# Performance work log

Measured on AMD Instinct MI355X. Metric: run time of the kernel, lower is better.

## Reference

```python
import jax, jax.numpy as jnp
import numpy as np

NUM_RBF = 64
CUTOFF = 5.0
N_GRAPHS = 64


def _rbf_expand(d):
    # Gaussian RBF expansion on [0, CUTOFF] with cosine cutoff envelope.
    mus = jnp.linspace(0.0, CUTOFF, NUM_RBF, dtype=d.dtype)  # [M]
    gamma = (NUM_RBF / CUTOFF) ** 2  # 1 / spacing^2
    fc = 0.5 * (jnp.cos(jnp.pi * d / CUTOFF) + 1.0) * (d < CUTOFF)  # [E]
    return jnp.exp(-gamma * (d[:, None] - mus[None, :]) ** 2) * fc[:, None]  # [E,M]


def setup_inputs() -> dict:
    key = jax.random.key(0)
    k0, k1, k2, k3, k4, k5 = jax.random.split(key, 6)
    N, E, T = 50000, 1600000, 25
    pos = jax.random.normal(k0, (N, 3), jnp.float32) * 3.0
    edge_index = jax.random.randint(k1, (2, E), 0, N)
    atom_types = jax.random.randint(k2, (N,), 0, T)
    batch = jnp.sort(jax.random.randint(k3, (N,), 0, N_GRAPHS))
    rbf_params = jax.random.normal(k4, (T, T, NUM_RBF), jnp.float32)
    radial_filters = jax.random.uniform(k5, (T, T, NUM_RBF), jnp.float32)
    return {
        "pos": pos,
        "rbf_params": rbf_params,
        "radial_filters": radial_filters,
        "edge_index": edge_index,
        "atom_types": atom_types,
        "batch": batch,
    }


def reference(pos, rbf_params, radial_filters, edge_index, atom_types, batch):
    src, dst = edge_index[0], edge_index[1]
    # distances (no cell shifts)
    diff = pos[dst] - pos[src]                       # [E,3]
    d = jnp.sqrt(jnp.sum(diff * diff, axis=-1) + 1e-12)  # [E]
    # type-pair lookup with canonical ordering (sender <= receiver)
    s = atom_types[src]
    r = atom_types[dst]
    lo = jnp.minimum(s, r)
    hi = jnp.maximum(s, r)
    params = rbf_params[lo, hi]        # [E,M]
    filt = radial_filters[lo, hi]      # [E,M] (already in [0,1])
    expn = _rbf_expand(d) * filt       # filtered RBF expansion
    e_edge = jnp.sum(expn * params, axis=1)  # [E]
    # reduce per-edge energies to per-graph energies
    bmap = batch[src]
    energy = jax.ops.segment_sum(e_edge, bmap, num_segments=N_GRAPHS)  # [G]
    return energy
```

## Files before the change

### kernel.cpp

```cpp
#include <hip/hip_runtime.h>
#include <math.h>

#define NUM_RBF 64
#define N_GRAPHS 64

typedef int   int4v   __attribute__((ext_vector_type(4)));
typedef float float4v __attribute__((ext_vector_type(4)));


__global__ __launch_bounds__(256) void prologue_kernel(
    const float4v* __restrict__ p, const float4v* __restrict__ f,
    float4v* __restrict__ C, int n4,
    const float* __restrict__ pos, const int* __restrict__ types,
    const int* __restrict__ batch, float4v* __restrict__ rec, int N)
{
    int i = blockIdx.x * blockDim.x + threadIdx.x;
    if (i < n4) C[i] = p[i] * f[i];
    if (i < N) {
        int bits = (types[i] & 0xFF) | ((batch[i] & 0xFF) << 8);
        float4v r = { pos[3 * i], pos[3 * i + 1], pos[3 * i + 2],
                      __int_as_float(bits) };
        rec[i] = r;
    }
}

#define CUTOFF_F      5.0f
#define GAMMA_F       163.84f
#define SPACING_F     (float)(5.0 / 63.0)
#define INV_SPACING_F (float)(63.0 / 5.0)
#define PI_OVER_C_F   (float)(3.14159265358979323846 / 5.0)
#define TWO_GAMMA_S_F (float)(2.0 * 163.84 * 5.0 / 63.0)
#define LN_V          (-(64.0 / 63.0) * (64.0 / 63.0))
#define V_1           (float)exp(LN_V)
#define V_2           (float)exp(2.0 * LN_V)

__device__ __forceinline__ void edge_body(
    float4v rs, float4v rd, const float4v* __restrict__ C4, int T,
    float* __restrict__ bins)
{
    const float dx = rd.x - rs.x;
    const float dy = rd.y - rs.y;
    const float dz = rd.z - rs.z;
    const float d  = sqrtf(dx * dx + dy * dy + dz * dz + 1e-12f);
    if (d >= CUTOFF_F) return;

    const int sb = __float_as_int(rs.w);
    const int db = __float_as_int(rd.w);
    const int ts = sb & 0xFF;
    const int td = db & 0xFF;
    const int lo = min(ts, td);
    const int hi = max(ts, td);
    const int base = (lo * T + hi) * NUM_RBF;

    const float c = d * INV_SPACING_F;
    int a0 = ((int)floorf(c - 3.5f)) & ~3;
    a0 = max(0, min(NUM_RBF - 12, a0));

    const float4v* w = C4 + ((base + a0) >> 2);
    const float4v w0 = w[0], w1 = w[1], w2 = w[2];

    const float delta = d - (float)a0 * SPACING_F;
    const float d5 = delta - 5.0f * SPACING_F;
    const float t5 = __expf(-GAMMA_F * d5 * d5);
    const float x  = TWO_GAMMA_S_F * d5;
    const float u  = __expf(x);
    const float ui = __expf(-x);

    float acc = w1.y * t5;
    float t = t5, m = u * V_1;
    t *= m;  acc += w1.z * t;  m *= V_2;
    t *= m;  acc += w1.w * t;  m *= V_2;
    t *= m;  acc += w2.x * t;  m *= V_2;
    t *= m;  acc += w2.y * t;  m *= V_2;
    t *= m;  acc += w2.z * t;  m *= V_2;
    t *= m;  acc += w2.w * t;
    t = t5;  m = ui * V_1;
    t *= m;  acc += w1.x * t;  m *= V_2;
    t *= m;  acc += w0.w * t;  m *= V_2;
    t *= m;  acc += w0.z * t;  m *= V_2;
    t *= m;  acc += w0.y * t;  m *= V_2;
    t *= m;  acc += w0.x * t;

    const float fc = 0.5f * (__cosf(PI_OVER_C_F * d) + 1.0f);
    atomicAdd(&bins[(sb >> 8) & 0xFF], acc * fc);
}

__global__ __launch_bounds__(256) void edge_energy_kernel(
    const int*     __restrict__ edge_index,
    const float4v* __restrict__ rec,
    const float4v* __restrict__ C4,
    float*         __restrict__ partial,
    int E, int T)
{
    __shared__ float bins[N_GRAPHS];
    for (int i = threadIdx.x; i < N_GRAPHS; i += blockDim.x) bins[i] = 0.0f;
    __syncthreads();

    const int nfull  = E >> 2;
    const int stride = gridDim.x * blockDim.x;
    const int gid    = blockIdx.x * blockDim.x + threadIdx.x;

    for (int q = gid; q < nfull; q += stride) {
        const int e0 = q << 2;
        const int4v sv = __builtin_nontemporal_load(
            (const int4v*)(edge_index + e0));
        const int4v tv = __builtin_nontemporal_load(
            (const int4v*)(edge_index + E + e0));

        const float4v rs0 = rec[sv.x], rd0 = rec[tv.x];
        const float4v rs1 = rec[sv.y], rd1 = rec[tv.y];
        const float4v rs2 = rec[sv.z], rd2 = rec[tv.z];
        const float4v rs3 = rec[sv.w], rd3 = rec[tv.w];

        edge_body(rs0, rd0, C4, T, bins);
        edge_body(rs1, rd1, C4, T, bins);
        edge_body(rs2, rd2, C4, T, bins);
        edge_body(rs3, rd3, C4, T, bins);
    }

    if (gid == 0) {
        for (int e = nfull << 2; e < E; ++e) {
            const float4v rs = rec[edge_index[e]];
            const float4v rd = rec[edge_index[E + e]];
            edge_body(rs, rd, C4, T, bins);
        }
    }

    __syncthreads();
    for (int i = threadIdx.x; i < N_GRAPHS; i += blockDim.x)
        partial[blockIdx.x * N_GRAPHS + i] = bins[i];
}

__global__ __launch_bounds__(256) void reduce_kernel(
    const float* __restrict__ partial, float* __restrict__ out, int nblocks)
{
    const int g = blockIdx.x;
    float s = 0.0f;
    for (int i = threadIdx.x; i < nblocks; i += blockDim.x)
        s += partial[i * N_GRAPHS + g];

    for (int off = 32; off > 0; off >>= 1)
        s += __shfl_down(s, off, 64);

    __shared__ float red[4];
    const int wave = threadIdx.x >> 6;
    const int lane = threadIdx.x & 63;
    if (lane == 0) red[wave] = s;
    __syncthreads();
    if (threadIdx.x == 0)
        out[g] = red[0] + red[1] + red[2] + red[3];
}

extern "C" void kernel_launch(void* const* d_in, const int* in_sizes, int n_in,
                              void* d_out, int out_size, void* d_ws, size_t ws_size,
                              hipStream_t stream) {
    const float* pos            = (const float*)d_in[0];
    const float* rbf_params     = (const float*)d_in[1];
    const float* radial_filters = (const float*)d_in[2];
    const int*   edge_index     = (const int*)d_in[3];
    const int*   atom_types     = (const int*)d_in[4];
    const int*   batch          = (const int*)d_in[5];
    float*       out            = (float*)d_out;

    const int E = in_sizes[3] / 2;
    const int N = in_sizes[4];
    int T = 1;
    while ((T + 1) * (T + 1) * NUM_RBF <= in_sizes[1]) ++T;
    const int tbl_elems = T * T * NUM_RBF;

    float*   Ctab    = (float*)d_ws;
    float4v* recs    = (float4v*)((char*)d_ws + ((size_t)tbl_elems * 4 + 255) / 256 * 256);
    float*   partial = (float*)((char*)recs + (size_t)N * 16);

    const int nq = E >> 2;
    int nblocks = (nq + 255) / 256;
    const size_t part_off = (size_t)((char*)partial - (char*)d_ws);
    const size_t avail = (ws_size > part_off) ? (ws_size - part_off) : 0;
    const int maxb = (int)(avail / (N_GRAPHS * sizeof(float)));
    if (nblocks > maxb) nblocks = maxb > 0 ? maxb : 1;
    if (nblocks < 1) nblocks = 1;

    const int pro_n = max(tbl_elems / 4, N);
    prologue_kernel<<<(pro_n + 255) / 256, 256, 0, stream>>>(
        (const float4v*)rbf_params, (const float4v*)radial_filters,
        (float4v*)Ctab, tbl_elems / 4, pos, atom_types, batch, recs, N);
    edge_energy_kernel<<<nblocks, 256, 0, stream>>>(
        edge_index, recs, (const float4v*)Ctab, partial, E, T);
    reduce_kernel<<<N_GRAPHS, 256, 0, stream>>>(partial, out, nblocks);
}
```

Measured before the change: 94.91 us.

## Compact in-cutoff edges into shared-memory queue before RBF evaluation

The edge loop is split into two phases. Each thread first computes squared distances and pushes the surviving edges (d² < cutoff²) into an LDS queue, using a wave ballot, mbcnt prefix and one atomic per wave. Then all 256 threads evaluate the RBF window densely from that queue. The aim is to remove lane divergence, since only a fraction of edges pass the cutoff. The cost is extra block-wide barriers per iteration, LDS traffic, and a packed type-pair/graph metadata format that assumes T*T < 1024 and fewer than 64 graphs.

```diff
diff --git a/kernel.cpp b/kernel.cpp
--- a/kernel.cpp
+++ b/kernel.cpp
@@ -3,6 +3,7 @@
 
 #define NUM_RBF 64
 #define N_GRAPHS 64
+#define QCAP     1032
 
 typedef int   int4v   __attribute__((ext_vector_type(4)));
 typedef float float4v __attribute__((ext_vector_type(4)));
@@ -24,7 +25,7 @@
     }
 }
 
-#define CUTOFF_F      5.0f
+#define CUTOFF2_F     25.0f
 #define GAMMA_F       163.84f
 #define SPACING_F     (float)(5.0 / 63.0)
 #define INV_SPACING_F (float)(63.0 / 5.0)
@@ -34,23 +35,13 @@
 #define V_1           (float)exp(LN_V)
 #define V_2           (float)exp(2.0 * LN_V)
 
-__device__ __forceinline__ void edge_body(
-    float4v rs, float4v rd, const float4v* __restrict__ C4, int T,
+__device__ __forceinline__ void window_body(
+    float d2, int meta, const float4v* __restrict__ C4,
     float* __restrict__ bins)
 {
-    const float dx = rd.x - rs.x;
-    const float dy = rd.y - rs.y;
-    const float dz = rd.z - rs.z;
-    const float d  = sqrtf(dx * dx + dy * dy + dz * dz + 1e-12f);
-    if (d >= CUTOFF_F) return;
-
-    const int sb = __float_as_int(rs.w);
-    const int db = __float_as_int(rd.w);
-    const int ts = sb & 0xFF;
-    const int td = db & 0xFF;
-    const int lo = min(ts, td);
-    const int hi = max(ts, td);
-    const int base = (lo * T + hi) * NUM_RBF;
+    const float d    = sqrtf(d2);
+    const int   base = (meta & 1023) << 6;
+    const int   bin  = meta >> 10;
 
     const float c = d * INV_SPACING_F;
     int a0 = ((int)floorf(c - 3.5f)) & ~3;
@@ -82,7 +73,39 @@
     t *= m;  acc += w0.x * t;
 
     const float fc = 0.5f * (__cosf(PI_OVER_C_F * d) + 1.0f);
-    atomicAdd(&bins[(sb >> 8) & 0xFF], acc * fc);
+    atomicAdd(&bins[bin], acc * fc);
+}
+
+__device__ __forceinline__ void push_body(
+    float4v rs, float4v rd, int T,
+    float* __restrict__ qd, int* __restrict__ qm, int* __restrict__ qcnt)
+{
+    const float dx = rd.x - rs.x;
+    const float dy = rd.y - rs.y;
+    const float dz = rd.z - rs.z;
+    const float d2 = dx * dx + dy * dy + dz * dz + 1e-12f;
+    const bool alive = d2 < CUTOFF2_F;
+
+    const unsigned long long mask = __ballot(alive);
+    if (alive) {
+        const int sb = __float_as_int(rs.w);
+        const int ts = sb & 0xFF;
+        const int td = __float_as_int(rd.w) & 0xFF;
+        const int lo = min(ts, td);
+        const int hi = max(ts, td);
+        const int meta = (lo * T + hi) | (((sb >> 8) & 0x3F) << 10);
+
+        const int prefix = __builtin_amdgcn_mbcnt_hi(
+            (unsigned)(mask >> 32),
+            __builtin_amdgcn_mbcnt_lo((unsigned)mask, 0));
+        const int first = __ffsll((unsigned long long)mask) - 1;
+        int off = 0;
+        if (((int)(threadIdx.x & 63)) == first)
+            off = atomicAdd(qcnt, (int)__popcll(mask));
+        off = __shfl(off, first, 64);
+        qd[off + prefix] = d2;
+        qm[off + prefix] = meta;
+    }
 }
 
 __global__ __launch_bounds__(256) void edge_energy_kernel(
@@ -93,41 +116,65 @@
     int E, int T)
 {
     __shared__ float bins[N_GRAPHS];
-    for (int i = threadIdx.x; i < N_GRAPHS; i += blockDim.x) bins[i] = 0.0f;
+    __shared__ float qd[QCAP];
+    __shared__ int   qm[QCAP];
+    __shared__ int   qcnt;
+
+    const int tid = threadIdx.x;
+    for (int i = tid; i < N_GRAPHS; i += blockDim.x) bins[i] = 0.0f;
+    if (tid == 0) qcnt = 0;
     __syncthreads();
 
-    const int nfull  = E >> 2;
-    const int stride = gridDim.x * blockDim.x;
-    const int gid    = blockIdx.x * blockDim.x + threadIdx.x;
-
-    for (int q = gid; q < nfull; q += stride) {
-        const int e0 = q << 2;
-        const int4v sv = __builtin_nontemporal_load(
-            (const int4v*)(edge_index + e0));
-        const int4v tv = __builtin_nontemporal_load(
-            (const int4v*)(edge_index + E + e0));
-
-        const float4v rs0 = rec[sv.x], rd0 = rec[tv.x];
-        const float4v rs1 = rec[sv.y], rd1 = rec[tv.y];
-        const float4v rs2 = rec[sv.z], rd2 = rec[tv.z];
-        const float4v rs3 = rec[sv.w], rd3 = rec[tv.w];
-
-        edge_body(rs0, rd0, C4, T, bins);
-        edge_body(rs1, rd1, C4, T, bins);
-        edge_body(rs2, rd2, C4, T, bins);
-        edge_body(rs3, rd3, C4, T, bins);
-    }
-
-    if (gid == 0) {
+    const int nfull = E >> 2;
+
+    if (blockIdx.x == 0 && tid == 0) {
         for (int e = nfull << 2; e < E; ++e) {
             const float4v rs = rec[edge_index[e]];
             const float4v rd = rec[edge_index[E + e]];
-            edge_body(rs, rd, C4, T, bins);
+            const float dx = rd.x - rs.x, dy = rd.y - rs.y, dz = rd.z - rs.z;
+            const float d2 = dx * dx + dy * dy + dz * dz + 1e-12f;
+            if (d2 < CUTOFF2_F) {
+                const int sb = __float_as_int(rs.w);
+                const int ts = sb & 0xFF;
+                const int td = __float_as_int(rd.w) & 0xFF;
+                const int meta = (min(ts, td) * T + max(ts, td))
+                               | (((sb >> 8) & 0x3F) << 10);
+                window_body(d2, meta, C4, bins);
+            }
         }
     }
 
-    __syncthreads();
-    for (int i = threadIdx.x; i < N_GRAPHS; i += blockDim.x)
+    const int bstride = gridDim.x * blockDim.x;
+    for (int q0 = blockIdx.x * blockDim.x; q0 < nfull; q0 += bstride) {
+        const int q = q0 + tid;
+        if (q < nfull) {
+            const int e0 = q << 2;
+            const int4v sv = __builtin_nontemporal_load(
+                (const int4v*)(edge_index + e0));
+            const int4v tv = __builtin_nontemporal_load(
+                (const int4v*)(edge_index + E + e0));
+
+            const float4v rs0 = rec[sv.x], rd0 = rec[tv.x];
+            const float4v rs1 = rec[sv.y], rd1 = rec[tv.y];
+            const float4v rs2 = rec[sv.z], rd2 = rec[tv.z];
+            const float4v rs3 = rec[sv.w], rd3 = rec[tv.w];
+
+            push_body(rs0, rd0, T, qd, qm, &qcnt);
+            push_body(rs1, rd1, T, qd, qm, &qcnt);
+            push_body(rs2, rd2, T, qd, qm, &qcnt);
+            push_body(rs3, rd3, T, qd, qm, &qcnt);
+        }
+
+        __syncthreads();
+        const int n = qcnt;
+        __syncthreads();
+        if (tid == 0) qcnt = 0;
+        for (int i = tid; i < n; i += 256)
+            window_body(qd[i], qm[i], C4, bins);
+        __syncthreads();
+    }
+
+    for (int i = tid; i < N_GRAPHS; i += blockDim.x)
         partial[blockIdx.x * N_GRAPHS + i] = bins[i];
 }
 
```

After: 97.14 us. 1.02x slower.

## Shrink RBF window to 8 terms, test squared cutoff, drop reduce kernel

Applied to the files above, without the earlier changes.

The Gaussian window shrinks from 12 terms to 8 terms, one-sided from a0, which cuts one float4 load and one exp per edge. The cutoff test now uses the squared distance so sqrt runs only for edges that pass. The separate reduce kernel is removed: each block atomically adds its shared bins into the output, which the prologue zeroes. This saves a launch and the partial-buffer traffic, but the narrower window truncates more Gaussian tails, which may reduce accuracy.

```diff
diff --git a/kernel.cpp b/kernel.cpp
--- a/kernel.cpp
+++ b/kernel.cpp
@@ -12,7 +12,8 @@
     const float4v* __restrict__ p, const float4v* __restrict__ f,
     float4v* __restrict__ C, int n4,
     const float* __restrict__ pos, const int* __restrict__ types,
-    const int* __restrict__ batch, float4v* __restrict__ rec, int N)
+    const int* __restrict__ batch, float4v* __restrict__ rec, int N,
+    float* __restrict__ out)
 {
     int i = blockIdx.x * blockDim.x + threadIdx.x;
     if (i < n4) C[i] = p[i] * f[i];
@@ -22,9 +23,10 @@
                       __int_as_float(bits) };
         rec[i] = r;
     }
+    if (i < N_GRAPHS) out[i] = 0.0f;
 }
 
-#define CUTOFF_F      5.0f
+#define CUTOFF2_F     25.0f
 #define GAMMA_F       163.84f
 #define SPACING_F     (float)(5.0 / 63.0)
 #define INV_SPACING_F (float)(63.0 / 5.0)
@@ -41,45 +43,37 @@
     const float dx = rd.x - rs.x;
     const float dy = rd.y - rs.y;
     const float dz = rd.z - rs.z;
-    const float d  = sqrtf(dx * dx + dy * dy + dz * dz + 1e-12f);
-    if (d >= CUTOFF_F) return;
+    const float d2 = dx * dx + dy * dy + dz * dz + 1e-12f;
+    if (d2 >= CUTOFF2_F) return;
 
+    const float d = sqrtf(d2);
     const int sb = __float_as_int(rs.w);
-    const int db = __float_as_int(rd.w);
     const int ts = sb & 0xFF;
-    const int td = db & 0xFF;
+    const int td = __float_as_int(rd.w) & 0xFF;
     const int lo = min(ts, td);
     const int hi = max(ts, td);
     const int base = (lo * T + hi) * NUM_RBF;
 
     const float c = d * INV_SPACING_F;
-    int a0 = ((int)floorf(c - 3.5f)) & ~3;
-    a0 = max(0, min(NUM_RBF - 12, a0));
+    int a0 = ((int)floorf(c - 1.5f)) & ~3;
+    a0 = max(0, min(NUM_RBF - 8, a0));
 
     const float4v* w = C4 + ((base + a0) >> 2);
-    const float4v w0 = w[0], w1 = w[1], w2 = w[2];
+    const float4v w0 = w[0], w1 = w[1];
 
     const float delta = d - (float)a0 * SPACING_F;
-    const float d5 = delta - 5.0f * SPACING_F;
-    const float t5 = __expf(-GAMMA_F * d5 * d5);
-    const float x  = TWO_GAMMA_S_F * d5;
-    const float u  = __expf(x);
-    const float ui = __expf(-x);
+    float t = __expf(-GAMMA_F * delta * delta);
+    const float u = __expf(TWO_GAMMA_S_F * delta);
+    float m = u * V_1;
 
-    float acc = w1.y * t5;
-    float t = t5, m = u * V_1;
-    t *= m;  acc += w1.z * t;  m *= V_2;
-    t *= m;  acc += w1.w * t;  m *= V_2;
-    t *= m;  acc += w2.x * t;  m *= V_2;
-    t *= m;  acc += w2.y * t;  m *= V_2;
-    t *= m;  acc += w2.z * t;  m *= V_2;
-    t *= m;  acc += w2.w * t;
-    t = t5;  m = ui * V_1;
-    t *= m;  acc += w1.x * t;  m *= V_2;
-    t *= m;  acc += w0.w * t;  m *= V_2;
-    t *= m;  acc += w0.z * t;  m *= V_2;
-    t *= m;  acc += w0.y * t;  m *= V_2;
-    t *= m;  acc += w0.x * t;
+    float acc = w0.x * t;
+    t *= m;  m *= V_2;  acc += w0.y * t;
+    t *= m;  m *= V_2;  acc += w0.z * t;
+    t *= m;  m *= V_2;  acc += w0.w * t;
+    t *= m;  m *= V_2;  acc += w1.x * t;
+    t *= m;  m *= V_2;  acc += w1.y * t;
+    t *= m;  m *= V_2;  acc += w1.z * t;
+    t *= m;            acc += w1.w * t;
 
     const float fc = 0.5f * (__cosf(PI_OVER_C_F * d) + 1.0f);
     atomicAdd(&bins[(sb >> 8) & 0xFF], acc * fc);
@@ -89,16 +83,17 @@
     const int*     __restrict__ edge_index,
     const float4v* __restrict__ rec,
     const float4v* __restrict__ C4,
-    float*         __restrict__ partial,
+    float*         __restrict__ out,
     int E, int T)
 {
     __shared__ float bins[N_GRAPHS];
-    for (int i = threadIdx.x; i < N_GRAPHS; i += blockDim.x) bins[i] = 0.0f;
+    const int tid = threadIdx.x;
+    for (int i = tid; i < N_GRAPHS; i += blockDim.x) bins[i] = 0.0f;
     __syncthreads();
 
     const int nfull  = E >> 2;
     const int stride = gridDim.x * blockDim.x;
-    const int gid    = blockIdx.x * blockDim.x + threadIdx.x;
+    const int gid    = blockIdx.x * blockDim.x + tid;
 
     for (int q = gid; q < nfull; q += stride) {
         const int e0 = q << 2;
@@ -127,28 +122,7 @@
     }
 
     __syncthreads();
-    for (int i = threadIdx.x; i < N_GRAPHS; i += blockDim.x)
-        partial[blockIdx.x * N_GRAPHS + i] = bins[i];
-}
-
-__global__ __launch_bounds__(256) void reduce_kernel(
-    const float* __restrict__ partial, float* __restrict__ out, int nblocks)
-{
-    const int g = blockIdx.x;
-    float s = 0.0f;
-    for (int i = threadIdx.x; i < nblocks; i += blockDim.x)
-        s += partial[i * N_GRAPHS + g];
-
-    for (int off = 32; off > 0; off >>= 1)
-        s += __shfl_down(s, off, 64);
-
-    __shared__ float red[4];
-    const int wave = threadIdx.x >> 6;
-    const int lane = threadIdx.x & 63;
-    if (lane == 0) red[wave] = s;
-    __syncthreads();
-    if (threadIdx.x == 0)
-        out[g] = red[0] + red[1] + red[2] + red[3];
+    if (tid < N_GRAPHS) atomicAdd(&out[tid], bins[tid]);
 }
 
 extern "C" void kernel_launch(void* const* d_in, const int* in_sizes, int n_in,
@@ -168,23 +142,17 @@
     while ((T + 1) * (T + 1) * NUM_RBF <= in_sizes[1]) ++T;
     const int tbl_elems = T * T * NUM_RBF;
 
-    float*   Ctab    = (float*)d_ws;
-    float4v* recs    = (float4v*)((char*)d_ws + ((size_t)tbl_elems * 4 + 255) / 256 * 256);
-    float*   partial = (float*)((char*)recs + (size_t)N * 16);
+    float*   Ctab = (float*)d_ws;
+    float4v* recs = (float4v*)((char*)d_ws + ((size_t)tbl_elems * 4 + 255) / 256 * 256);
 
     const int nq = E >> 2;
     int nblocks = (nq + 255) / 256;
-    const size_t part_off = (size_t)((char*)partial - (char*)d_ws);
-    const size_t avail = (ws_size > part_off) ? (ws_size - part_off) : 0;
-    const int maxb = (int)(avail / (N_GRAPHS * sizeof(float)));
-    if (nblocks > maxb) nblocks = maxb > 0 ? maxb : 1;
     if (nblocks < 1) nblocks = 1;
 
     const int pro_n = max(tbl_elems / 4, N);
     prologue_kernel<<<(pro_n + 255) / 256, 256, 0, stream>>>(
         (const float4v*)rbf_params, (const float4v*)radial_filters,
-        (float4v*)Ctab, tbl_elems / 4, pos, atom_types, batch, recs, N);
+        (float4v*)Ctab, tbl_elems / 4, pos, atom_types, batch, recs, N, out);
     edge_energy_kernel<<<nblocks, 256, 0, stream>>>(
-        edge_index, recs, (const float4v*)Ctab, partial, E, T);
-    reduce_kernel<<<N_GRAPHS, 256, 0, stream>>>(partial, out, nblocks);
+        edge_index, recs, (const float4v*)Ctab, out, E, T);
 }
```

Measured after the change: 118.8 us. 25.2% more time.
